# Performance work log

Hardware: AMD Instinct MI355X
Metric: run time of the kernel (lower is better)

## Reference

```python
import jax, jax.numpy as jnp
import numpy as np

SOS_TOKEN = 1
B, H, V, T = 64, 1024, 32000, 40
INPUT_SIZE = 4096


def setup_inputs() -> dict:
    key = jax.random.key(0)
    ks = jax.random.split(key, 12)
    s = 1.0 / np.sqrt(H)
    return {
        "output": jax.random.normal(ks[0], (B, INPUT_SIZE), jnp.float32),
        "h0": jax.random.normal(ks[1], (1, B, H), jnp.float32),
        "c0": jax.random.normal(ks[2], (1, B, H), jnp.float32),
        "target_outputs": jax.random.randint(ks[3], (B, T), 0, V, jnp.int64),
        "target_lengths": jnp.full((B,), T, jnp.int64),
        "embed": jax.random.normal(ks[4], (V, H), jnp.float32),
        "w_ih": jax.random.uniform(ks[5], (4 * H, H), jnp.float32, -s, s),
        "w_hh": jax.random.uniform(ks[6], (4 * H, H), jnp.float32, -s, s),
        "b_ih": jax.random.uniform(ks[7], (4 * H,), jnp.float32, -s, s),
        "b_hh": jax.random.uniform(ks[8], (4 * H,), jnp.float32, -s, s),
        "w_out": jax.random.uniform(ks[9], (V, H), jnp.float32, -s, s),
        "b_out": jax.random.uniform(ks[10], (V,), jnp.float32, -s, s),
    }


def _lstm_cell(x, h, c, w_ih, w_hh, b_ih, b_hh):
    # PyTorch LSTMCell math; gate order i, f, g, o
    gates = x @ w_ih.T + b_ih + h @ w_hh.T + b_hh  # [B, 4H]
    i, f, g, o = jnp.split(gates, 4, axis=-1)
    c2 = jax.nn.sigmoid(f) * c + jax.nn.sigmoid(i) * jnp.tanh(g)
    h2 = jax.nn.sigmoid(o) * jnp.tanh(c2)
    return h2, c2


def reference(output, h0, c0, target_outputs, target_lengths,
              embed, w_ih, w_hh, b_ih, b_hh, w_out, b_out):
    batch = output.shape[0]
    max_lens = int(jnp.max(target_lengths))
    h, c = h0[0], c0[0]  # num_layers=1 -> [B, H]

    # Initial symbol = SOS; initial dec_o = W(embed(SOS)) (no LSTM), as in torch code
    symbol0 = jnp.full((batch,), SOS_TOKEN, dtype=target_outputs.dtype)
    dec_o0 = embed[symbol0] @ w_out.T + b_out  # [B, V]

    def step(carry, _):
        symbol, dec_o, h, c = carry
        # emit current (symbol, dec_o), then decode next
        x = embed[symbol]  # [B, H]
        h2, c2 = _lstm_cell(x, h, c, w_ih, w_hh, b_ih, b_hh)
        dec2 = h2 @ w_out.T + b_out  # [B, V]
        sym2 = jnp.argmax(dec2, axis=-1).astype(symbol.dtype)  # greedy topk(1)
        return (sym2, dec2, h2, c2), (symbol, dec_o)
    (_, _, _, _), (symbols, decs) = jax.lax.scan(
        step, (symbol0, dec_o0, h, c), None, length=max_lens)

    decoder_outs = jnp.transpose(decs, (1, 0, 2))  # [B, T, V]
    symbol_outs = jnp.transpose(symbols, (1, 0))   # [B, T]
    return decoder_outs, symbol_outs
```

## Files before the change

### kernel.cpp

```cpp
#include <hip/hip_runtime.h>

#define Bdim 64
#define Hdim 1024
#define Vdim 32000
#define Tdim 40

typedef __bf16 bf16x8 __attribute__((ext_vector_type(8)));
typedef float  f32x4  __attribute__((ext_vector_type(4)));
typedef unsigned short u16x8 __attribute__((ext_vector_type(8)));
static_assert(sizeof(bf16x8) == 16, "bf16x8 must be 16B");

__device__ __forceinline__ unsigned long long pack_key(float f, int v) {
    unsigned u = __float_as_uint(f);
    u = (u & 0x80000000u) ? ~u : (u | 0x80000000u);
    return ((unsigned long long)u << 32) | (unsigned long long)(0xFFFFFFFFu - (unsigned)v);
}

__device__ __forceinline__ int decode_key(unsigned long long key) {
    return (int)(0xFFFFFFFFu - (unsigned)(key & 0xFFFFFFFFull));
}

__device__ __forceinline__ void gll16(const void* g, void* l) {
    __builtin_amdgcn_global_load_lds(
        (const __attribute__((address_space(1))) void*)g,
        (__attribute__((address_space(3))) void*)l, 16, 0, 0);
}

#define VMW(n) asm volatile("s_waitcnt vmcnt(" #n ")" ::: "memory")

struct BSplit { unsigned short h, m, l; };

__device__ __forceinline__ BSplit bsplit3v(float x) {
    __bf16 h = (__bf16)x;  float r  = x - (float)h;
    __bf16 m = (__bf16)r;  float r2 = r - (float)m;
    __bf16 l = (__bf16)r2;
    BSplit s;
    s.h = __builtin_bit_cast(unsigned short, h);
    s.m = __builtin_bit_cast(unsigned short, m);
    s.l = __builtin_bit_cast(unsigned short, l);
    return s;
}

__device__ __forceinline__ void bsplit3(float x, unsigned short& a, unsigned short& b,
                                        unsigned short& c) {
    BSplit s = bsplit3v(x);
    a = s.h; b = s.m; c = s.l;
}

template<bool AM>
__global__ __launch_bounds__(512, 1) void k_logits(
    const float* __restrict__ w_out,
    const unsigned short* __restrict__ ah, const unsigned short* __restrict__ am,
    const unsigned short* __restrict__ al,
    const float* __restrict__ b_out, float* __restrict__ out,
    unsigned long long* __restrict__ slots)
{
    constexpr int NW = 8, NCH = 32;
    constexpr int WBYTES = NW * 2048;
    constexpr int BUFSZ  = WBYTES + 12288;
    extern __shared__ __align__(16) unsigned char smem[];
    __shared__ unsigned long long red[NW][4][16];

    const int tid  = threadIdx.x;
    const int lane = tid & 63;
    const int wid  = tid >> 6;
    const int vb   = blockIdx.x * 128;

    const unsigned char* Wb = (const unsigned char*)(w_out + (size_t)vb * Hdim);
    const unsigned char* Apb[3] = {(const unsigned char*)ah, (const unsigned char*)am,
                                   (const unsigned char*)al};

    f32x4 acc[4] = {};

    const int ar = tid >> 2, as = tid & 3;
    const int aswz = as ^ ((ar >> 1) & 3);
    const size_t asrc_off = (size_t)ar * 2048 + (size_t)aswz * 16;

    auto stage = [&](int bufidx, int ch) {
        unsigned char* bb = smem + bufidx * BUFSZ;
        const size_t kb4 = (size_t)ch * 128;
#pragma unroll
        for (int s = 0; s < 2; s++) {
            int gg = tid + 512 * s;
            int rw = gg >> 3, cc = gg & 7;
            int sg = cc ^ (rw & 7);
            gll16(Wb + (size_t)rw * 4096 + kb4 + (size_t)sg * 16,
                  bb + ((wid * 64 + 512 * s) << 4));
        }
        if (tid < 256) {
            const size_t kb2 = (size_t)ch * 64;
#pragma unroll
            for (int pl = 0; pl < 3; pl++)
                gll16(Apb[pl] + asrc_off + kb2, bb + WBYTES + pl * 4096 + (wid << 10));
        }
    };

    stage(0, 0); stage(1, 1); stage(2, 2);

    const int col  = lane & 15;
    const int kg   = lane >> 4;
    const int wrow = wid * 16 + col;
    const int wg0  = (2 * kg) ^ (wrow & 7);
    const int wg1  = (2 * kg + 1) ^ (wrow & 7);

#pragma unroll 2
    for (int ch = 0; ch < NCH; ch++) {
        if (ch + 3 < NCH) stage((ch + 3) & 3, ch + 3);
        const int k = (NCH - 1 - ch < 3) ? (NCH - 1 - ch) : 3;
        if (wid < 4) {
            if (k == 3) VMW(15); else if (k == 2) VMW(10);
            else if (k == 1) VMW(5); else VMW(0);
        } else {
            if (k == 3) VMW(6); else if (k == 2) VMW(4);
            else if (k == 1) VMW(2); else VMW(0);
        }
        __builtin_amdgcn_sched_barrier(0);
        __builtin_amdgcn_s_barrier();
        __builtin_amdgcn_sched_barrier(0);

        const unsigned char* base = smem + (ch & 3) * BUFSZ;

        const unsigned char* Wr = base + wrow * 128;
        f32x4 w0 = *(const f32x4*)(Wr + (wg0 << 4));
        f32x4 w1 = *(const f32x4*)(Wr + (wg1 << 4));
        bf16x8 whi, wmid, wlo;
#pragma unroll
        for (int j = 0; j < 4; j++) {
            float x0 = w0[j], x1 = w1[j];
            __bf16 a0 = (__bf16)x0; float r0 = x0 - (float)a0;
            __bf16 b0 = (__bf16)r0; float q0 = r0 - (float)b0;
            whi[j] = a0; wmid[j] = b0; wlo[j] = (__bf16)q0;
            __bf16 a1 = (__bf16)x1; float r1 = x1 - (float)a1;
            __bf16 b1 = (__bf16)r1; float q1 = r1 - (float)b1;
            whi[4 + j] = a1; wmid[4 + j] = b1; wlo[4 + j] = (__bf16)q1;
        }
#pragma unroll
        for (int bt = 0; bt < 4; bt++) {
            const int arow = bt * 16 + col;
            const unsigned char* Ar = base + WBYTES + arow * 64
                                    + ((kg ^ ((arow >> 1) & 3)) << 4);
            bf16x8 ahi = *(const bf16x8*)Ar;
            bf16x8 ami = *(const bf16x8*)(Ar + 4096);
            bf16x8 alo = *(const bf16x8*)(Ar + 8192);
            acc[bt] = __builtin_amdgcn_mfma_f32_16x16x32_bf16(whi,  ahi, acc[bt], 0, 0, 0);
            acc[bt] = __builtin_amdgcn_mfma_f32_16x16x32_bf16(whi,  ami, acc[bt], 0, 0, 0);
            acc[bt] = __builtin_amdgcn_mfma_f32_16x16x32_bf16(wmid, ahi, acc[bt], 0, 0, 0);
            acc[bt] = __builtin_amdgcn_mfma_f32_16x16x32_bf16(whi,  alo, acc[bt], 0, 0, 0);
            acc[bt] = __builtin_amdgcn_mfma_f32_16x16x32_bf16(wlo,  ahi, acc[bt], 0, 0, 0);
            acc[bt] = __builtin_amdgcn_mfma_f32_16x16x32_bf16(wmid, ami, acc[bt], 0, 0, 0);
        }
        __builtin_amdgcn_sched_barrier(0);
        __builtin_amdgcn_s_barrier();
        __builtin_amdgcn_sched_barrier(0);
    }

    const int ncol = vb + wid * 16 + kg * 4;
    f32x4 bv = *(const f32x4*)(b_out + ncol);

    unsigned long long bk[4];
#pragma unroll
    for (int bt = 0; bt < 4; bt++) {
        const int b = bt * 16 + col;
        float* op = out + (size_t)b * ((size_t)Tdim * Vdim) + ncol;
        f32x4 vv;
        unsigned long long best = 0ull;
#pragma unroll
        for (int r = 0; r < 4; r++) {
            float val = acc[bt][r] + bv[r];
            vv[r] = val;
            if (AM) {
                unsigned long long key = pack_key(val, ncol + r);
                if (key > best) best = key;
            }
        }
        *(f32x4*)op = vv;
        bk[bt] = best;
    }

    if constexpr (AM) {
#pragma unroll
        for (int bt = 0; bt < 4; bt++) {
            unsigned long long k = bk[bt];
            unsigned long long o = __shfl_xor(k, 16, 64); if (o > k) k = o;
            o = __shfl_xor(k, 32, 64);                    if (o > k) k = o;
            if (lane < 16) red[wid][bt][lane] = k;
        }
        __syncthreads();
        if (tid < 64) {
            const int bt = tid >> 4, c = tid & 15;
            unsigned long long k = red[0][bt][c];
#pragma unroll
            for (int w = 1; w < NW; w++)
                if (red[w][bt][c] > k) k = red[w][bt][c];
            atomicMax(&slots[bt * 16 + c], k);
        }
    }
}

template<int NW, int NCH, bool BIAS, bool GATHER>
__device__ __forceinline__ void mm_core(
    unsigned char* sm,
    const float* __restrict__ W,
    const unsigned short* __restrict__ Ah,
    const unsigned short* __restrict__ Am,
    const unsigned short* __restrict__ Al,
    const float* __restrict__ Gsrc,
    const unsigned long long* __restrict__ slots_in, int tstep,
    float* __restrict__ sym_dst,
    int n0, const float* __restrict__ bias,
    float* __restrict__ out, size_t out_bstride)
{
    constexpr int NT     = NW * 64;
    constexpr int WBYTES = NW * 2048;
    constexpr int BUFSZ  = WBYTES + 12288;

    const int tid  = threadIdx.x;
    const int lane = tid & 63;
    const int wid  = tid >> 6;

    f32x4 acc[4] = {};

    const unsigned char* Wb = (const unsigned char*)W;
    const unsigned char* Apb[3] = {(const unsigned char*)Ah, (const unsigned char*)Am,
                                   (const unsigned char*)Al};

    const int ar = tid >> 2, as = tid & 3;
    const int aswz = as ^ ((ar >> 1) & 3);
    const size_t asrc_off = (size_t)ar * 2048 + (size_t)aswz * 16;
    const size_t aldst    = (size_t)ar * 64 + (size_t)aswz * 16;

    const float* grow = nullptr;
    if constexpr (GATHER) {
        if (tid < 256) {
            int symv = 1;
            if (tstep > 0) {
                unsigned long long key = slots_in[ar];
                symv = decode_key(key);
                if (sym_dst != nullptr && as == 0)
                    sym_dst[ar * Tdim + tstep] = (float)symv;
            }
            grow = Gsrc + (size_t)symv * 1024 + as * 8;
        }
    }

    auto stage = [&](int bufidx, int ch) {
        unsigned char* bb = sm + bufidx * BUFSZ;
        const size_t kb4 = (size_t)ch * 128;
#pragma unroll
        for (int s = 0; s < 2; s++) {
            int gg = tid + NT * s;
            int rw = gg >> 3, cc = gg & 7;
            int sg = cc ^ (rw & 7);
            gll16(Wb + (size_t)rw * 4096 + kb4 + (size_t)sg * 16,
                  bb + ((wid * 64 + NT * s) << 4));
        }
        if constexpr (GATHER) {
            if (tid < 256) {
                const float* p = grow + ch * 32;
                float4 f0 = *(const float4*)(p);
                float4 f1 = *(const float4*)(p + 4);
                u16x8 vh, vm, vl;
                BSplit s0 = bsplit3v(f0.x); vh[0] = s0.h; vm[0] = s0.m; vl[0] = s0.l;
                BSplit s1 = bsplit3v(f0.y); vh[1] = s1.h; vm[1] = s1.m; vl[1] = s1.l;
                BSplit s2 = bsplit3v(f0.z); vh[2] = s2.h; vm[2] = s2.m; vl[2] = s2.l;
                BSplit s3 = bsplit3v(f0.w); vh[3] = s3.h; vm[3] = s3.m; vl[3] = s3.l;
                BSplit s4 = bsplit3v(f1.x); vh[4] = s4.h; vm[4] = s4.m; vl[4] = s4.l;
                BSplit s5 = bsplit3v(f1.y); vh[5] = s5.h; vm[5] = s5.m; vl[5] = s5.l;
                BSplit s6 = bsplit3v(f1.z); vh[6] = s6.h; vm[6] = s6.m; vl[6] = s6.l;
                BSplit s7 = bsplit3v(f1.w); vh[7] = s7.h; vm[7] = s7.m; vl[7] = s7.l;
                *(u16x8*)(bb + WBYTES + aldst)        = vh;
                *(u16x8*)(bb + WBYTES + 4096 + aldst) = vm;
                *(u16x8*)(bb + WBYTES + 8192 + aldst) = vl;
            }
        } else {
            if (tid < 256) {
                const size_t kb2 = (size_t)ch * 64;
#pragma unroll
                for (int pl = 0; pl < 3; pl++)
                    gll16(Apb[pl] + asrc_off + kb2,
                          bb + WBYTES + pl * 4096 + (wid << 10));
            }
        }
    };

    stage(0, 0);
    __syncthreads();

    const int col  = lane & 15;
    const int kg   = lane >> 4;
    const int wrow = wid * 16 + col;
    const int wg0  = (2 * kg) ^ (wrow & 7);
    const int wg1  = (2 * kg + 1) ^ (wrow & 7);

#pragma unroll 2
    for (int ch = 0; ch < NCH; ch++) {
        if (ch + 1 < NCH) stage((ch + 1) & 1, ch + 1);
        unsigned char* base = sm + (ch & 1) * BUFSZ;

        const unsigned char* Wr = base + wrow * 128;
        f32x4 w0 = *(const f32x4*)(Wr + (wg0 << 4));
        f32x4 w1 = *(const f32x4*)(Wr + (wg1 << 4));
        bf16x8 whi, wmid, wlo;
#pragma unroll
        for (int j = 0; j < 4; j++) {
            float x0 = w0[j], x1 = w1[j];
            __bf16 a0 = (__bf16)x0; float r0 = x0 - (float)a0;
            __bf16 b0 = (__bf16)r0; float q0 = r0 - (float)b0;
            whi[j] = a0; wmid[j] = b0; wlo[j] = (__bf16)q0;
            __bf16 a1 = (__bf16)x1; float r1 = x1 - (float)a1;
            __bf16 b1 = (__bf16)r1; float q1 = r1 - (float)b1;
            whi[4 + j] = a1; wmid[4 + j] = b1; wlo[4 + j] = (__bf16)q1;
        }
#pragma unroll
        for (int bt = 0; bt < 4; bt++) {
            const int arow = bt * 16 + col;
            const unsigned char* Ar = base + WBYTES + arow * 64
                                    + ((kg ^ ((arow >> 1) & 3)) << 4);
            bf16x8 ahi = *(const bf16x8*)Ar;
            bf16x8 ami = *(const bf16x8*)(Ar + 4096);
            bf16x8 alo = *(const bf16x8*)(Ar + 8192);
            acc[bt] = __builtin_amdgcn_mfma_f32_16x16x32_bf16(whi,  ahi, acc[bt], 0, 0, 0);
            acc[bt] = __builtin_amdgcn_mfma_f32_16x16x32_bf16(whi,  ami, acc[bt], 0, 0, 0);
            acc[bt] = __builtin_amdgcn_mfma_f32_16x16x32_bf16(wmid, ahi, acc[bt], 0, 0, 0);
            acc[bt] = __builtin_amdgcn_mfma_f32_16x16x32_bf16(whi,  alo, acc[bt], 0, 0, 0);
            acc[bt] = __builtin_amdgcn_mfma_f32_16x16x32_bf16(wlo,  ahi, acc[bt], 0, 0, 0);
            acc[bt] = __builtin_amdgcn_mfma_f32_16x16x32_bf16(wmid, ami, acc[bt], 0, 0, 0);
        }
        __syncthreads();
    }

    const int ncol = n0 + wid * 16 + kg * 4;
    f32x4 bv = {};
    if (BIAS) bv = *(const f32x4*)(bias + ncol);

#pragma unroll
    for (int bt = 0; bt < 4; bt++) {
        const int b = bt * 16 + col;
        float* op = out + (size_t)b * out_bstride + ncol;
        f32x4 vv;
#pragma unroll
        for (int r = 0; r < 4; r++) {
            float val = acc[bt][r];
            if (BIAS) val += bv[r];
            vv[r] = val;
        }
        *(f32x4*)op = vv;
    }
}

__global__ __launch_bounds__(256, 2) void k_gates(
    const float* __restrict__ w_ih, const float* __restrict__ w_hh,
    const unsigned short* __restrict__ hh, const unsigned short* __restrict__ hm,
    const unsigned short* __restrict__ hl,
    const float* __restrict__ embed, unsigned long long* __restrict__ slots,
    int t, float* __restrict__ sym_out, float* __restrict__ gp)
{
    __shared__ __align__(16) unsigned char smem[2][20480];
    const int nbi = blockIdx.x, y = blockIdx.y, z = blockIdx.z;
    const float* W = (y ? w_hh : w_ih) + (size_t)nbi * 65536 + z * 256;
    float* gout = gp + (size_t)(y * 4 + z) * (Bdim * 4096);
    if (y)
        mm_core<4, 8, false, false>(&smem[0][0], W,
            hh + z * 256, hm + z * 256, hl + z * 256, nullptr, nullptr, t, nullptr,
            nbi * 64, nullptr, gout, 4096);
    else
        mm_core<4, 8, false, true>(&smem[0][0], W,
            nullptr, nullptr, nullptr, embed + z * 256, slots, t,
            ((nbi == 0 && z == 0) ? sym_out : nullptr),
            nbi * 64, nullptr, gout, 4096);
}

__global__ void k_cell(const float* __restrict__ gp, const float* __restrict__ b_ih,
                       const float* __restrict__ b_hh, float* __restrict__ cbuf,
                       unsigned short* __restrict__ hh, unsigned short* __restrict__ hm,
                       unsigned short* __restrict__ hl,
                       unsigned long long* __restrict__ slots)
{
    const int idx = blockIdx.x * 256 + threadIdx.x;
    const int b = idx >> 10, k = idx & 1023;
    const size_t S = (size_t)Bdim * 4096;
    const size_t base = (size_t)b * 4096;
    float g[4];
#pragma unroll
    for (int q = 0; q < 4; q++) {
        size_t o = base + q * 1024 + k;
        float s = gp[o];
#pragma unroll
        for (int i = 1; i < 8; i++) s += gp[i * S + o];
        g[q] = s + b_ih[q * 1024 + k] + b_hh[q * 1024 + k];
    }
    float si = 1.f / (1.f + expf(-g[0]));
    float sf = 1.f / (1.f + expf(-g[1]));
    float so = 1.f / (1.f + expf(-g[3]));
    float c  = cbuf[idx];
    float c2 = sf * c + si * tanhf(g[2]);
    float h2 = so * tanhf(c2);
    cbuf[idx] = c2;
    unsigned short hs, ms, ls;
    bsplit3(h2, hs, ms, ls);
    const size_t o = (size_t)b * 1024 + k;
    hh[o] = hs; hm[o] = ms; hl[o] = ls;
    if (idx < 64) slots[idx] = 0ull;
}

__global__ void k_init(const float* __restrict__ embed, const float* __restrict__ h0,
                       const float* __restrict__ c0,
                       unsigned short* __restrict__ xsh, unsigned short* __restrict__ xsm,
                       unsigned short* __restrict__ xsl,
                       unsigned short* __restrict__ hh, unsigned short* __restrict__ hm,
                       unsigned short* __restrict__ hl,
                       float* __restrict__ cbuf, float* __restrict__ sym_out,
                       unsigned long long* __restrict__ slots)
{
    const int b = blockIdx.x, t4 = threadIdx.x * 4;
    if (threadIdx.x == 0) { sym_out[b * Tdim] = 1.0f; slots[b] = 0ull; }
    const size_t o = (size_t)b * 1024 + t4;
    ushort4 hi4, mi4, lo4;

    float4 e = *(const float4*)(embed + 1024 + t4);
    bsplit3(e.x, hi4.x, mi4.x, lo4.x);
    bsplit3(e.y, hi4.y, mi4.y, lo4.y);
    bsplit3(e.z, hi4.z, mi4.z, lo4.z);
    bsplit3(e.w, hi4.w, mi4.w, lo4.w);
    *(ushort4*)(xsh + o) = hi4; *(ushort4*)(xsm + o) = mi4; *(ushort4*)(xsl + o) = lo4;

    float4 hv = *(const float4*)(h0 + (size_t)b * 1024 + t4);
    bsplit3(hv.x, hi4.x, mi4.x, lo4.x);
    bsplit3(hv.y, hi4.y, mi4.y, lo4.y);
    bsplit3(hv.z, hi4.z, mi4.z, lo4.z);
    bsplit3(hv.w, hi4.w, mi4.w, lo4.w);
    *(ushort4*)(hh + o) = hi4; *(ushort4*)(hm + o) = mi4; *(ushort4*)(hl + o) = lo4;

    float4 cv = *(const float4*)(c0 + (size_t)b * 1024 + t4);
    *(float4*)(cbuf + (size_t)b * 1024 + t4) = cv;
}

__global__ void k_symfinal(const unsigned long long* __restrict__ slots,
                           float* __restrict__ sym_out)
{
    const int b = threadIdx.x;
    sym_out[b * Tdim + (Tdim - 1)] = (float)decode_key(slots[b]);
}

extern "C" void kernel_launch(void* const* d_in, const int* in_sizes, int n_in,
                              void* d_out, int out_size, void* d_ws, size_t ws_size,
                              hipStream_t stream)
{
    const float* h0    = (const float*)d_in[1];
    const float* c0    = (const float*)d_in[2];
    const float* embed = (const float*)d_in[5];
    const float* w_ih  = (const float*)d_in[6];
    const float* w_hh  = (const float*)d_in[7];
    const float* b_ih  = (const float*)d_in[8];
    const float* b_hh  = (const float*)d_in[9];
    const float* w_out = (const float*)d_in[10];
    const float* b_out = (const float*)d_in[11];

    float* out = (float*)d_out;
    float* sym_out = out + (size_t)Bdim * Tdim * Vdim;

    unsigned short* hh  = (unsigned short*)d_ws;
    unsigned short* hm  = hh + (size_t)Bdim * 1024;
    unsigned short* hl  = hm + (size_t)Bdim * 1024;
    unsigned short* xsh = hl + (size_t)Bdim * 1024;
    unsigned short* xsm = xsh + (size_t)Bdim * 1024;
    unsigned short* xsl = xsm + (size_t)Bdim * 1024;
    float* cbuf = (float*)(xsl + (size_t)Bdim * 1024);
    float* gp   = cbuf + (size_t)Bdim * Hdim;
    unsigned long long* slots = (unsigned long long*)(gp + 8ull * Bdim * 4096);

    constexpr size_t LOGITS_LDS = 4 * 28672;

    k_init<<<Bdim, 256, 0, stream>>>(embed, h0, c0, xsh, xsm, xsl,
                                     hh, hm, hl, cbuf, sym_out, slots);

    k_logits<false><<<Vdim / 128, 512, LOGITS_LDS, stream>>>(w_out, xsh, xsm, xsl,
                                                             b_out, out, slots);

    for (int t = 0; t < Tdim - 1; t++) {
        k_gates<<<dim3(64, 2, 4), 256, 0, stream>>>(w_ih, w_hh, hh, hm, hl,
                                                    embed, slots, t, sym_out, gp);
        k_cell<<<Bdim * Hdim / 256, 256, 0, stream>>>(gp, b_ih, b_hh, cbuf,
                                                      hh, hm, hl, slots);
        k_logits<true><<<Vdim / 128, 512, LOGITS_LDS, stream>>>(
            w_out, hh, hm, hl, b_out, out + (size_t)(t + 1) * Vdim, slots);
    }
    k_symfinal<<<1, 64, 0, stream>>>(slots, sym_out);
}
```

Before: 2.650 ms.

## Load activation operand directly to registers and double-buffer weights in LDS

```diff
diff --git a/kernel.cpp b/kernel.cpp
--- a/kernel.cpp
+++ b/kernel.cpp
@@ -25,8 +25,6 @@
         (const __attribute__((address_space(1))) void*)g,
         (__attribute__((address_space(3))) void*)l, 16, 0, 0);
 }
-
-#define VMW(n) asm volatile("s_waitcnt vmcnt(" #n ")" ::: "memory")
 
 struct BSplit { unsigned short h, m, l; };
 
@@ -57,8 +55,7 @@
 {
     constexpr int NW = 8, NCH = 32;
     constexpr int WBYTES = NW * 2048;
-    constexpr int BUFSZ  = WBYTES + 12288;
-    extern __shared__ __align__(16) unsigned char smem[];
+    __shared__ __align__(16) unsigned char smem[2][WBYTES];
     __shared__ unsigned long long red[NW][4][16];
 
     const int tid  = threadIdx.x;
@@ -67,17 +64,14 @@
     const int vb   = blockIdx.x * 128;
 
     const unsigned char* Wb = (const unsigned char*)(w_out + (size_t)vb * Hdim);
-    const unsigned char* Apb[3] = {(const unsigned char*)ah, (const unsigned char*)am,
-                                   (const unsigned char*)al};
 
     f32x4 acc[4] = {};
 
-    const int ar = tid >> 2, as = tid & 3;
-    const int aswz = as ^ ((ar >> 1) & 3);
-    const size_t asrc_off = (size_t)ar * 2048 + (size_t)aswz * 16;
-
-    auto stage = [&](int bufidx, int ch) {
-        unsigned char* bb = smem + bufidx * BUFSZ;
+    const int col = lane & 15;
+    const int kg  = lane >> 4;
+
+    auto stageW = [&](int bufidx, int ch) {
+        unsigned char* bb = smem[bufidx];
         const size_t kb4 = (size_t)ch * 128;
 #pragma unroll
         for (int s = 0; s < 2; s++) {
@@ -87,39 +81,23 @@
             gll16(Wb + (size_t)rw * 4096 + kb4 + (size_t)sg * 16,
                   bb + ((wid * 64 + 512 * s) << 4));
         }
-        if (tid < 256) {
-            const size_t kb2 = (size_t)ch * 64;
-#pragma unroll
-            for (int pl = 0; pl < 3; pl++)
-                gll16(Apb[pl] + asrc_off + kb2, bb + WBYTES + pl * 4096 + (wid << 10));
-        }
     };
 
-    stage(0, 0); stage(1, 1); stage(2, 2);
-
-    const int col  = lane & 15;
-    const int kg   = lane >> 4;
+    auto loadA = [&](bf16x8* a, int ch) {
+#pragma unroll
+        for (int bt = 0; bt < 4; bt++) {
+            const size_t ro = (size_t)(bt * 16 + col) * 1024 + (size_t)ch * 32 + kg * 8;
+            a[bt * 3 + 0] = *(const bf16x8*)(ah + ro);
+            a[bt * 3 + 1] = *(const bf16x8*)(am + ro);
+            a[bt * 3 + 2] = *(const bf16x8*)(al + ro);
+        }
+    };
+
     const int wrow = wid * 16 + col;
     const int wg0  = (2 * kg) ^ (wrow & 7);
     const int wg1  = (2 * kg + 1) ^ (wrow & 7);
 
-#pragma unroll 2
-    for (int ch = 0; ch < NCH; ch++) {
-        if (ch + 3 < NCH) stage((ch + 3) & 3, ch + 3);
-        const int k = (NCH - 1 - ch < 3) ? (NCH - 1 - ch) : 3;
-        if (wid < 4) {
-            if (k == 3) VMW(15); else if (k == 2) VMW(10);
-            else if (k == 1) VMW(5); else VMW(0);
-        } else {
-            if (k == 3) VMW(6); else if (k == 2) VMW(4);
-            else if (k == 1) VMW(2); else VMW(0);
-        }
-        __builtin_amdgcn_sched_barrier(0);
-        __builtin_amdgcn_s_barrier();
-        __builtin_amdgcn_sched_barrier(0);
-
-        const unsigned char* base = smem + (ch & 3) * BUFSZ;
-
+    auto compute = [&](const unsigned char* base, const bf16x8* a) {
         const unsigned char* Wr = base + wrow * 128;
         f32x4 w0 = *(const f32x4*)(Wr + (wg0 << 4));
         f32x4 w1 = *(const f32x4*)(Wr + (wg1 << 4));
@@ -136,12 +114,9 @@
         }
 #pragma unroll
         for (int bt = 0; bt < 4; bt++) {
-            const int arow = bt * 16 + col;
-            const unsigned char* Ar = base + WBYTES + arow * 64
-                                    + ((kg ^ ((arow >> 1) & 3)) << 4);
-            bf16x8 ahi = *(const bf16x8*)Ar;
-            bf16x8 ami = *(const bf16x8*)(Ar + 4096);
-            bf16x8 alo = *(const bf16x8*)(Ar + 8192);
+            bf16x8 ahi = a[bt * 3 + 0];
+            bf16x8 ami = a[bt * 3 + 1];
+            bf16x8 alo = a[bt * 3 + 2];
             acc[bt] = __builtin_amdgcn_mfma_f32_16x16x32_bf16(whi,  ahi, acc[bt], 0, 0, 0);
             acc[bt] = __builtin_amdgcn_mfma_f32_16x16x32_bf16(whi,  ami, acc[bt], 0, 0, 0);
             acc[bt] = __builtin_amdgcn_mfma_f32_16x16x32_bf16(wmid, ahi, acc[bt], 0, 0, 0);
@@ -149,9 +124,21 @@
             acc[bt] = __builtin_amdgcn_mfma_f32_16x16x32_bf16(wlo,  ahi, acc[bt], 0, 0, 0);
             acc[bt] = __builtin_amdgcn_mfma_f32_16x16x32_bf16(wmid, ami, acc[bt], 0, 0, 0);
         }
-        __builtin_amdgcn_sched_barrier(0);
-        __builtin_amdgcn_s_barrier();
-        __builtin_amdgcn_sched_barrier(0);
+    };
+
+    bf16x8 aA[12], aB[12];
+    loadA(aA, 0);
+    stageW(0, 0);
+    __syncthreads();
+
+    for (int ch = 0; ch < NCH; ch += 2) {
+        stageW(1, ch + 1);
+        loadA(aB, ch + 1);
+        compute(smem[0], aA);
+        __syncthreads();
+        if (ch + 2 < NCH) { stageW(0, ch + 2); loadA(aA, ch + 2); }
+        compute(smem[1], aB);
+        __syncthreads();
     }
 
     const int ncol = vb + wid * 16 + kg * 4;
@@ -469,21 +456,20 @@
     float* gp   = cbuf + (size_t)Bdim * Hdim;
     unsigned long long* slots = (unsigned long long*)(gp + 8ull * Bdim * 4096);
 
-    constexpr size_t LOGITS_LDS = 4 * 28672;
-
     k_init<<<Bdim, 256, 0, stream>>>(embed, h0, c0, xsh, xsm, xsl,
                                      hh, hm, hl, cbuf, sym_out, slots);
 
-    k_logits<false><<<Vdim / 128, 512, LOGITS_LDS, stream>>>(w_out, xsh, xsm, xsl,
-                                                             b_out, out, slots);
+    k_logits<false><<<Vdim / 128, 512, 0, stream>>>(w_out, xsh, xsm, xsl,
+                                                    b_out, out, slots);
 
     for (int t = 0; t < Tdim - 1; t++) {
         k_gates<<<dim3(64, 2, 4), 256, 0, stream>>>(w_ih, w_hh, hh, hm, hl,
                                                     embed, slots, t, sym_out, gp);
         k_cell<<<Bdim * Hdim / 256, 256, 0, stream>>>(gp, b_ih, b_hh, cbuf,
                                                       hh, hm, hl, slots);
-        k_logits<true><<<Vdim / 128, 512, LOGITS_LDS, stream>>>(
-            w_out, hh, hm, hl, b_out, out + (size_t)(t + 1) * Vdim, slots);
+        k_logits<true><<<Vdim / 128, 512, 0, stream>>>(w_out, hh, hm, hl,
+                                                       b_out, out + (size_t)(t + 1) * Vdim,
+                                                       slots);
     }
     k_symfinal<<<1, 64, 0, stream>>>(slots, sym_out);
 }
```

After: 5.425 ms. 2.05x slower.
